# Kernel tuning notes

Hardware: AMD Instinct MI355X
Metric: run time of the kernel (lower is better)

## Reference

```python
import jax, jax.numpy as jnp
import numpy as np

HEADS, DIM_HEAD, LANDMARKS, PINV_ITERS = 8, 64, 256, 6
DIM = 512
KERNEL = 33  # residual depthwise conv kernel size (lucidrains NystromAttention default)
EPS = 1e-5   # torch LayerNorm eps


def setup_inputs() -> dict:
    key = jax.random.key(0)
    ks = jax.random.split(key, 4)
    b, n = 4, 8192  # n divisible by LANDMARKS -> no padding branch
    w = lambda k, shape: jax.random.normal(k, shape, dtype=jnp.float32) * 0.02
    return {
        "x": jax.random.normal(ks[0], (b, n, DIM), dtype=jnp.float32),
        "ln_gamma": jnp.ones((DIM,), jnp.float32),
        "ln_beta": jnp.zeros((DIM,), jnp.float32),
        "w_qkv": w(ks[1], (DIM, 3 * HEADS * DIM_HEAD)),   # to_qkv, no bias
        "w_out": w(ks[2], (HEADS * DIM_HEAD, DIM)),
        "b_out": jnp.zeros((DIM,), jnp.float32),
        "res_kernel": w(ks[3], (HEADS, 1, KERNEL, 1)),    # Conv2d(heads, heads, (33,1), groups=heads)
    }


def _moore_penrose_pinv(a, iters):
    # iterative Moore-Penrose pseudoinverse (lucidrains)
    abs_a = jnp.abs(a)
    col = abs_a.sum(-1).max()  # global max, matching torch.max(col)
    row = abs_a.sum(-2).max()
    z = jnp.swapaxes(a, -1, -2) / (col * row)
    I = jnp.eye(a.shape[-1], dtype=a.dtype)
    for _ in range(iters):
        az = a @ z
        z = 0.25 * z @ (13.0 * I - az @ (15.0 * I - az @ (7.0 * I - az)))
    return z


def reference(x, ln_gamma, ln_beta, w_qkv, w_out, b_out, res_kernel):
    b, n, d = x.shape
    h, dh, m = HEADS, DIM_HEAD, LANDMARKS
    # --- LayerNorm ---
    mu = x.mean(-1, keepdims=True)
    var = ((x - mu) ** 2).mean(-1, keepdims=True)
    xn = (x - mu) * jax.lax.rsqrt(var + EPS) * ln_gamma + ln_beta
    # --- qkv projection ---
    qkv = xn @ w_qkv                                   # (b, n, 3*h*dh)
    q, k, v = jnp.split(qkv, 3, axis=-1)
    to_heads = lambda t: t.reshape(b, n, h, dh).transpose(0, 2, 1, 3)  # (b, h, n, dh)
    q, k, v = to_heads(q), to_heads(k), to_heads(v)
    q = q * (dh ** -0.5)
    # --- landmark pooling (mean over groups of l tokens) ---
    l = n // m
    q_l = q.reshape(b, h, m, l, dh).mean(3)            # (b, h, m, dh)
    k_l = k.reshape(b, h, m, l, dh).mean(3)
    # --- three similarity matrices + softmaxes ---
    attn1 = jax.nn.softmax(jnp.einsum('bhnd,bhmd->bhnm', q, k_l), axis=-1)    # (b,h,n,m)
    attn2 = jax.nn.softmax(jnp.einsum('bhid,bhjd->bhij', q_l, k_l), axis=-1)  # (b,h,m,m)
    attn3 = jax.nn.softmax(jnp.einsum('bhmd,bhnd->bhmn', q_l, k), axis=-1)    # (b,h,m,n)
    out = (attn1 @ _moore_penrose_pinv(attn2, PINV_ITERS)) @ (attn3 @ v)      # (b,h,n,dh)
    # --- depthwise residual conv over sequence dim (groups = heads) ---
    res = jax.lax.conv_general_dilated(
        v, res_kernel, window_strides=(1, 1),
        padding=((KERNEL // 2, KERNEL // 2), (0, 0)),
        dimension_numbers=('NCHW', 'OIHW', 'NCHW'),
        feature_group_count=h)
    out = out + res
    # --- merge heads, output projection, outer residual ---
    out = out.transpose(0, 2, 1, 3).reshape(b, n, h * dh)
    att = out @ w_out + b_out
    return x + att
```

## Files before the change

kernel.cpp:

```cpp
#include <hip/hip_runtime.h>
#include <math.h>

#define NB 4
#define NSEQ 8192
#define DMODEL 512
#define NHEADS 8
#define DHEAD 64
#define NLM 256
#define LTOK 32
#define NBH 32
#define KCONV 33
#define CH3 8

typedef unsigned short bf16_t;
typedef __attribute__((ext_vector_type(8))) short bf16x8;
typedef __attribute__((ext_vector_type(4))) float f32x4;

__device__ __forceinline__ float bf2f(bf16_t u) {
  return __uint_as_float(((unsigned)u) << 16);
}
__device__ __forceinline__ bf16_t f2bf(float f) {
  unsigned u = __float_as_uint(f);
  return (bf16_t)((u + 0x7fffu + ((u >> 16) & 1u)) >> 16);
}
__device__ __forceinline__ void bfpair(unsigned u, float& lo, float& hi) {
  lo = __uint_as_float(u << 16);
  hi = __uint_as_float(u & 0xffff0000u);
}

__global__ __launch_bounds__(256) void ln_kernel(const float* __restrict__ x,
    const float* __restrict__ gamma, const float* __restrict__ beta,
    bf16_t* __restrict__ xn) {
  int row = blockIdx.x * 4 + (threadIdx.x >> 6);
  int lane = threadIdx.x & 63;
  const float4* xr = reinterpret_cast<const float4*>(x + (size_t)row * DMODEL);
  float4 a0 = xr[lane];
  float4 a1 = xr[lane + 64];
  float s  = a0.x + a0.y + a0.z + a0.w + a1.x + a1.y + a1.z + a1.w;
  float s2 = a0.x*a0.x + a0.y*a0.y + a0.z*a0.z + a0.w*a0.w
           + a1.x*a1.x + a1.y*a1.y + a1.z*a1.z + a1.w*a1.w;
  #pragma unroll
  for (int off = 32; off; off >>= 1) {
// ... 215 lines not shown
}

__global__ void colrow_kernel(const float* __restrict__ a2, unsigned int* __restrict__ scal) {
  int bh = blockIdx.x & 31, mode = blockIdx.x >> 5;
  int t = threadIdx.x;
  const float* Ab = a2 + (size_t)bh * NLM * NLM;
  float sum = 0.f;
  if (mode == 0) { for (int j = 0; j < NLM; ++j) sum += fabsf(Ab[(size_t)t * NLM + j]); }
  else           { for (int i2 = 0; i2 < NLM; ++i2) sum += fabsf(Ab[(size_t)i2 * NLM + t]); }
  __shared__ float red[256];
  red[t] = sum; __syncthreads();
  for (int off = 128; off; off >>= 1) { if (t < off) red[t] = fmaxf(red[t], red[t + off]); __syncthreads(); }
  if (t == 0) atomicMax(&scal[mode], __float_as_uint(red[0]));
}

__global__ void zinit_kernel(const float* __restrict__ a2, const unsigned int* __restrict__ scal,
                             bf16_t* __restrict__ zb, bf16_t* __restrict__ a2b) {
  int idx = blockIdx.x * 256 + threadIdx.x;
  float inv = 1.0f / (__uint_as_float(scal[0]) * __uint_as_float(scal[1]));
  int j = idx & 255, i = (idx >> 8) & 255, bh = idx >> 16;
  zb[idx] = f2bf(a2[((size_t)bh * NLM + j) * NLM + i] * inv);
  a2b[idx] = f2bf(a2[idx]);
}

__global__ __launch_bounds__(256) void matmul256_b2b(bf16_t* __restrict__ C,
    const bf16_t* __restrict__ A, const bf16_t* __restrict__ Bm, float s, float alpha) {
  __shared__ __align__(16) bf16_t Ah[64][72];
  __shared__ __align__(16) bf16_t Bh[64][72];
  int bh = blockIdx.y;
  const bf16_t* Ab = A + (size_t)bh * NLM * NLM;
  const bf16_t* Bb = Bm + (size_t)bh * NLM * NLM;
  bf16_t* Cb = C + (size_t)bh * NLM * NLM;
  int rowB = (blockIdx.x >> 2) * 64, colB = (blockIdx.x & 3) * 64;
  int tid = threadIdx.x, w = tid >> 6, lane = tid & 63, tx = lane & 15, g = lane >> 4;
  int jj = tid >> 2, part = tid & 3;
  f32x4 acc[4] = {};
  for (int k0 = 0; k0 < NLM; k0 += 64) {
    {
      const uint4* ar = reinterpret_cast<const uint4*>(
          Ab + (size_t)(rowB + jj) * NLM + k0 + part * 16);
      *reinterpret_cast<uint4*>(&Ah[jj][part * 16]) = ar[0];
      *reinterpret_cast<uint4*>(&Ah[jj][part * 16 + 8]) = ar[1];
      const uint4* br = reinterpret_cast<const uint4*>(
          Bb + (size_t)(k0 + jj) * NLM + colB + part * 16);
      uint4 b0 = br[0], b1 = br[1];
      int d0 = part * 16;
      Bh[d0+ 0][jj] = (bf16_t)(b0.x & 0xffffu); Bh[d0+ 1][jj] = (bf16_t)(b0.x >> 16);
      Bh[d0+ 2][jj] = (bf16_t)(b0.y & 0xffffu); Bh[d0+ 3][jj] = (bf16_t)(b0.y >> 16);
      Bh[d0+ 4][jj] = (bf16_t)(b0.z & 0xffffu); Bh[d0+ 5][jj] = (bf16_t)(b0.z >> 16);
      Bh[d0+ 6][jj] = (bf16_t)(b0.w & 0xffffu); Bh[d0+ 7][jj] = (bf16_t)(b0.w >> 16);
      Bh[d0+ 8][jj] = (bf16_t)(b1.x & 0xffffu); Bh[d0+ 9][jj] = (bf16_t)(b1.x >> 16);
      Bh[d0+10][jj] = (bf16_t)(b1.y & 0xffffu); Bh[d0+11][jj] = (bf16_t)(b1.y >> 16);
      Bh[d0+12][jj] = (bf16_t)(b1.z & 0xffffu); Bh[d0+13][jj] = (bf16_t)(b1.z >> 16);
      Bh[d0+14][jj] = (bf16_t)(b1.w & 0xffffu); Bh[d0+15][jj] = (bf16_t)(b1.w >> 16);
    }
    __syncthreads();
    #pragma unroll
    for (int ks = 0; ks < 2; ++ks) {
      bf16x8 ah = *reinterpret_cast<const bf16x8*>(&Ah[w * 16 + tx][g * 8 + 32 * ks]);
      #pragma unroll
      for (int tn = 0; tn < 4; ++tn) {
        bf16x8 bhf = *reinterpret_cast<const bf16x8*>(&Bh[tn * 16 + tx][g * 8 + 32 * ks]);
        acc[tn] = __builtin_amdgcn_mfma_f32_16x16x32_bf16(ah, bhf, acc[tn], 0, 0, 0);
      }
    }
    __syncthreads();
  }
  #pragma unroll
  for (int tn = 0; tn < 4; ++tn) {
    int c = colB + tn * 16 + tx;
    #pragma unroll
    for (int r = 0; r < 4; ++r) {
      int rr = rowB + w * 16 + g * 4 + r;
      float aij = (s != 0.0f) ? bf2f(Ab[(size_t)rr * NLM + c]) : 0.0f;
      Cb[(size_t)rr * NLM + c] = f2bf(alpha * (s * aij - acc[tn][r]));
    }
  }
}

__global__ __launch_bounds__(256) void matmul256_b2f(float* __restrict__ C,
    const bf16_t* __restrict__ A, const bf16_t* __restrict__ Bm, float s, float alpha) {
  __shared__ __align__(16) bf16_t Ah[64][72];
  __shared__ __align__(16) bf16_t Bh[64][72];
  int bh = blockIdx.y;
  const bf16_t* Ab = A + (size_t)bh * NLM * NLM;
  const bf16_t* Bb = Bm + (size_t)bh * NLM * NLM;
  float* Cb = C + (size_t)bh * NLM * NLM;
  int rowB = (blockIdx.x >> 2) * 64, colB = (blockIdx.x & 3) * 64;
  int tid = threadIdx.x, w = tid >> 6, lane = tid & 63, tx = lane & 15, g = lane >> 4;
  int jj = tid >> 2, part = tid & 3;
  f32x4 acc[4] = {};
  for (int k0 = 0; k0 < NLM; k0 += 64) {
    {
      const uint4* ar = reinterpret_cast<const uint4*>(
          Ab + (size_t)(rowB + jj) * NLM + k0 + part * 16);
      *reinterpret_cast<uint4*>(&Ah[jj][part * 16]) = ar[0];
      *reinterpret_cast<uint4*>(&Ah[jj][part * 16 + 8]) = ar[1];
      const uint4* br = reinterpret_cast<const uint4*>(
          Bb + (size_t)(k0 + jj) * NLM + colB + part * 16);
      uint4 b0 = br[0], b1 = br[1];
      int d0 = part * 16;
      Bh[d0+ 0][jj] = (bf16_t)(b0.x & 0xffffu); Bh[d0+ 1][jj] = (bf16_t)(b0.x >> 16);
      Bh[d0+ 2][jj] = (bf16_t)(b0.y & 0xffffu); Bh[d0+ 3][jj] = (bf16_t)(b0.y >> 16);
      Bh[d0+ 4][jj] = (bf16_t)(b0.z & 0xffffu); Bh[d0+ 5][jj] = (bf16_t)(b0.z >> 16);
      Bh[d0+ 6][jj] = (bf16_t)(b0.w & 0xffffu); Bh[d0+ 7][jj] = (bf16_t)(b0.w >> 16);
      Bh[d0+ 8][jj] = (bf16_t)(b1.x & 0xffffu); Bh[d0+ 9][jj] = (bf16_t)(b1.x >> 16);
      Bh[d0+10][jj] = (bf16_t)(b1.y & 0xffffu); Bh[d0+11][jj] = (bf16_t)(b1.y >> 16);
      Bh[d0+12][jj] = (bf16_t)(b1.z & 0xffffu); Bh[d0+13][jj] = (bf16_t)(b1.z >> 16);
      Bh[d0+14][jj] = (bf16_t)(b1.w & 0xffffu); Bh[d0+15][jj] = (bf16_t)(b1.w >> 16);
    }
    __syncthreads();
    #pragma unroll
    for (int ks = 0; ks < 2; ++ks) {
      bf16x8 ah = *reinterpret_cast<const bf16x8*>(&Ah[w * 16 + tx][g * 8 + 32 * ks]);
      #pragma unroll
      for (int tn = 0; tn < 4; ++tn) {
        bf16x8 bhf = *reinterpret_cast<const bf16x8*>(&Bh[tn * 16 + tx][g * 8 + 32 * ks]);
        acc[tn] = __builtin_amdgcn_mfma_f32_16x16x32_bf16(ah, bhf, acc[tn], 0, 0, 0);
      }
    }
    __syncthreads();
  }
  #pragma unroll
  for (int tn = 0; tn < 4; ++tn) {
    int c = colB + tn * 16 + tx;
    #pragma unroll
    for (int r = 0; r < 4; ++r) {
      int rr = rowB + w * 16 + g * 4 + r;
      float aij = (s != 0.0f) ? bf2f(Ab[(size_t)rr * NLM + c]) : 0.0f;
      Cb[(size_t)rr * NLM + c] = alpha * (s * aij - acc[tn][r]);
    }
  }
}

__global__ __launch_bounds__(256) void matmul256_mfma(float* __restrict__ C,
    const float* __restrict__ A, const float* __restrict__ Bm, float s, float alpha) {
  __shared__ __align__(16) bf16_t Ah[64][72];
  __shared__ __align__(16) bf16_t Al[64][72];
  __shared__ __align__(16) bf16_t Bh[64][72];
  __shared__ __align__(16) bf16_t Bl[64][72];
  int bh = blockIdx.y;
  const float* Ab = A + (size_t)bh * NLM * NLM;
  const float* Bb = Bm + (size_t)bh * NLM * NLM;
  float* Cb = C + (size_t)bh * NLM * NLM;
  int rowB = (blockIdx.x >> 2) * 64, colB = (blockIdx.x & 3) * 64;
  int tid = threadIdx.x, w = tid >> 6, lane = tid & 63, tx = lane & 15, g = lane >> 4;
  f32x4 acc[4] = {};
  for (int k0 = 0; k0 < NLM; k0 += 64) {
    {
      int jj = tid >> 2, part = tid & 3;
      const float* ar = Ab + (size_t)(rowB + jj) * NLM + k0 + part * 16;
      #pragma unroll
      for (int e = 0; e < 16; ++e) {
        float xv = ar[e];
        unsigned u = __float_as_uint(xv);
        Ah[jj][part * 16 + e] = (bf16_t)(u >> 16);
        Al[jj][part * 16 + e] = f2bf(xv - __uint_as_float(u & 0xffff0000u));
      }
      const float* br = Bb + (size_t)(k0 + jj) * NLM + colB + part * 16;
      #pragma unroll
      for (int e = 0; e < 16; ++e) {
        float xv = br[e];
        unsigned u = __float_as_uint(xv);
        Bh[part * 16 + e][jj] = (bf16_t)(u >> 16);
        Bl[part * 16 + e][jj] = f2bf(xv - __uint_as_float(u & 0xffff0000u));
      }
    }
    __syncthreads();
    #pragma unroll
    for (int ks = 0; ks < 2; ++ks) {
      bf16x8 ah = *reinterpret_cast<const bf16x8*>(&Ah[w * 16 + tx][g * 8 + 32 * ks]);
      bf16x8 al = *reinterpret_cast<const bf16x8*>(&Al[w * 16 + tx][g * 8 + 32 * ks]);
      #pragma unroll
      for (int tn = 0; tn < 4; ++tn) {
        bf16x8 bhf = *reinterpret_cast<const bf16x8*>(&Bh[tn * 16 + tx][g * 8 + 32 * ks]);
        bf16x8 blf = *reinterpret_cast<const bf16x8*>(&Bl[tn * 16 + tx][g * 8 + 32 * ks]);
        acc[tn] = __builtin_amdgcn_mfma_f32_16x16x32_bf16(ah, bhf, acc[tn], 0, 0, 0);
        acc[tn] = __builtin_amdgcn_mfma_f32_16x16x32_bf16(ah, blf, acc[tn], 0, 0, 0);
        acc[tn] = __builtin_amdgcn_mfma_f32_16x16x32_bf16(al, bhf, acc[tn], 0, 0, 0);
      }
    }
    __syncthreads();
  }
  #pragma unroll
  for (int tn = 0; tn < 4; ++tn) {
    int c = colB + tn * 16 + tx;
    #pragma unroll
    for (int r = 0; r < 4; ++r) {
      int rr = rowB + w * 16 + g * 4 + r;
      float aij = (s != 0.0f) ? Ab[(size_t)rr * NLM + c] : 0.0f;
      Cb[(size_t)rr * NLM + c] = alpha * (s * aij - acc[tn][r]);
    }
  }
}

__global__ __launch_bounds__(256) void attn3v_mfma(const bf16_t* __restrict__ qlb,
    const bf16_t* __restrict__ k, const bf16_t* __restrict__ vT,
    float* __restrict__ Wpart, float* __restrict__ mlpart) {
  __shared__ __align__(16) bf16_t Qs[64][72];
  __shared__ __align__(16) bf16_t Ks[64][72];
  __shared__ __align__(16) bf16_t Vt[64][72];
  __shared__ __align__(16) bf16_t Ps[64][72];
  int chunk = blockIdx.x, lmt = blockIdx.y, bh = blockIdx.z;
  int tid = threadIdx.x;
  int w = tid >> 6, lane = tid & 63;
  int tx = lane & 15, g = lane >> 4;
  int lm0 = lmt * 64;
  int jj = tid >> 2, part = tid & 3;
  {
    const uint4* qr = reinterpret_cast<const uint4*>(
        qlb + ((size_t)bh * NLM + lm0 + jj) * DHEAD + part * 16);
    *reinterpret_cast<uint4*>(&Qs[jj][part * 16]) = qr[0];
    *reinterpret_cast<uint4*>(&Qs[jj][part * 16 + 8]) = qr[1];
  }
  f32x4 oacc[4] = {};
  float lreg[4] = {0.f, 0.f, 0.f, 0.f};
  const bf16_t* kb = k + (size_t)bh * NSEQ * DHEAD;
  const bf16_t* vtb = vT + (size_t)bh * DHEAD * NSEQ + (size_t)jj * NSEQ;
  __syncthreads();
  for (int it = 0; it < NSEQ / (CH3 * 64); ++it) {
    int n0 = chunk * (NSEQ / CH3) + it * 64;
    {
      const uint4* kr = reinterpret_cast<const uint4*>(kb + (size_t)(n0 + jj) * DHEAD + part * 16);
      *reinterpret_cast<uint4*>(&Ks[jj][part * 16]) = kr[0];
      *reinterpret_cast<uint4*>(&Ks[jj][part * 16 + 8]) = kr[1];
      const uint4* vr = reinterpret_cast<const uint4*>(vtb + n0 + part * 16);
      *reinterpret_cast<uint4*>(&Vt[jj][part * 16]) = vr[0];
      *reinterpret_cast<uint4*>(&Vt[jj][part * 16 + 8]) = vr[1];
    }
    __syncthreads();
    f32x4 sacc[4] = {};
    bf16x8 aq0 = *reinterpret_cast<const bf16x8*>(&Qs[w * 16 + tx][g * 8]);
    bf16x8 aq1 = *reinterpret_cast<const bf16x8*>(&Qs[w * 16 + tx][g * 8 + 32]);
    #pragma unroll
    for (int tn = 0; tn < 4; ++tn) {
      bf16x8 bk0 = *reinterpret_cast<const bf16x8*>(&Ks[tn * 16 + tx][g * 8]);
      bf16x8 bk1 = *reinterpret_cast<const bf16x8*>(&Ks[tn * 16 + tx][g * 8 + 32]);
      sacc[tn] = __builtin_amdgcn_mfma_f32_16x16x32_bf16(aq0, bk0, sacc[tn], 0, 0, 0);
      sacc[tn] = __builtin_amdgcn_mfma_f32_16x16x32_bf16(aq1, bk1, sacc[tn], 0, 0, 0);
    }
    #pragma unroll
    for (int r = 0; r < 4; ++r) {
      float p0 = __expf(sacc[0][r]);
      float p1 = __expf(sacc[1][r]);
      float p2 = __expf(sacc[2][r]);
      float p3 = __expf(sacc[3][r]);
      float ts = p0 + p1 + p2 + p3;
      #pragma unroll
      for (int off = 1; off < 16; off <<= 1) ts += __shfl_xor(ts, off);
      lreg[r] += ts;
      int prow = w * 16 + g * 4 + r;
      Ps[prow][tx]      = f2bf(p0);
      Ps[prow][tx + 16] = f2bf(p1);
      Ps[prow][tx + 32] = f2bf(p2);
      Ps[prow][tx + 48] = f2bf(p3);
    }
    __syncthreads();
    bf16x8 ap0 = *reinterpret_cast<const bf16x8*>(&Ps[w * 16 + tx][g * 8]);
    bf16x8 ap1 = *reinterpret_cast<const bf16x8*>(&Ps[w * 16 + tx][g * 8 + 32]);
    #pragma unroll
    for (int td = 0; td < 4; ++td) {
      bf16x8 bv0 = *reinterpret_cast<const bf16x8*>(&Vt[td * 16 + tx][g * 8]);
      bf16x8 bv1 = *reinterpret_cast<const bf16x8*>(&Vt[td * 16 + tx][g * 8 + 32]);
      oacc[td] = __builtin_amdgcn_mfma_f32_16x16x32_bf16(ap0, bv0, oacc[td], 0, 0, 0);
      oacc[td] = __builtin_amdgcn_mfma_f32_16x16x32_bf16(ap1, bv1, oacc[td], 0, 0, 0);
    }
    __syncthreads();
  }
  #pragma unroll
  for (int r = 0; r < 4; ++r) {
    size_t ob = ((size_t)(chunk * NBH + bh) * NLM + lm0 + w * 16 + g * 4 + r);
    #pragma unroll
    for (int td = 0; td < 4; ++td)
      Wpart[ob * DHEAD + tx + 16 * td] = oacc[td][r];
    if (tx == 0) { mlpart[ob * 2] = 0.f; mlpart[ob * 2 + 1] = lreg[r]; }
  }
}

// ... 4 lines not shown
  int s0 = idx >> 6;
  const int CHS = NBH * NLM;
  float M = -1e30f;
  #pragma unroll
  for (int c = 0; c < CH3; ++c) M = fmaxf(M, mlpart[((size_t)c * CHS + s0) * 2]);
  float L = 0.f, wv = 0.f;
  #pragma unroll
  for (int c = 0; c < CH3; ++c) {
    float e = __expf(mlpart[((size_t)c * CHS + s0) * 2] - M);
    L += mlpart[((size_t)c * CHS + s0) * 2 + 1] * e;
    wv += Wpart[((size_t)c * CHS + s0) * DHEAD + d] * e;
  }
  Wm[idx] = wv / L;
}

__global__ void zw_kernel(const float* __restrict__ z, const float* __restrict__ W,
                          bf16_t* __restrict__ Ub) {
  int idx = blockIdx.x * 256 + threadIdx.x;
  int d = idx & 63, i = (idx >> 6) & 255, bh = idx >> 14;
  const float* zr = z + ((size_t)bh * NLM + i) * NLM;
  const float* Wb = W + (size_t)bh * NLM * DHEAD + d;
  float acc = 0.f;
  for (int j = 0; j < NLM; ++j) acc += zr[j] * Wb[(size_t)j * DHEAD];
  Ub[idx] = f2bf(acc);
}

__global__ __launch_bounds__(256) void attn1_mfma(const bf16_t* __restrict__ q,
    const bf16_t* __restrict__ klb, const bf16_t* __restrict__ Ut,
    bf16_t* __restrict__ outp) {
  __shared__ __align__(16) bf16_t Qs[64][72];
  __shared__ __align__(16) bf16_t Ks[64][72];
  __shared__ __align__(16) bf16_t Vt[64][72];
  __shared__ __align__(16) bf16_t Ps[64][72];
  int nt = blockIdx.x, bh = blockIdx.y;
  int tid = threadIdx.x;
  int w = tid >> 6, lane = tid & 63;
  int tx = lane & 15, g = lane >> 4;
  int n0 = nt * 64;
  int b = bh >> 3, h = bh & 7;
  int jj = tid >> 2, part = tid & 3;
  {
    const uint4* qr = reinterpret_cast<const uint4*>(
        q + ((size_t)bh * NSEQ + n0 + jj) * DHEAD + part * 16);
    *reinterpret_cast<uint4*>(&Qs[jj][part * 16]) = qr[0];
    *reinterpret_cast<uint4*>(&Qs[jj][part * 16 + 8]) = qr[1];
  }
  f32x4 oacc[4] = {};
  float lreg[4] = {0.f, 0.f, 0.f, 0.f};
  const bf16_t* utb = Ut + (size_t)bh * DHEAD * NLM + (size_t)jj * NLM;
  __syncthreads();
  for (int it = 0; it < 4; ++it) {
    int lm0 = it * 64;
    {
      const uint4* kr = reinterpret_cast<const uint4*>(
          klb + ((size_t)bh * NLM + lm0 + jj) * DHEAD + part * 16);
      *reinterpret_cast<uint4*>(&Ks[jj][part * 16]) = kr[0];
      *reinterpret_cast<uint4*>(&Ks[jj][part * 16 + 8]) = kr[1];
      const uint4* ur = reinterpret_cast<const uint4*>(utb + lm0 + part * 16);
      *reinterpret_cast<uint4*>(&Vt[jj][part * 16]) = ur[0];
      *reinterpret_cast<uint4*>(&Vt[jj][part * 16 + 8]) = ur[1];
    }
    __syncthreads();
    f32x4 sacc[4] = {};
    bf16x8 aq0 = *reinterpret_cast<const bf16x8*>(&Qs[w * 16 + tx][g * 8]);
    bf16x8 aq1 = *reinterpret_cast<const bf16x8*>(&Qs[w * 16 + tx][g * 8 + 32]);
    #pragma unroll
    for (int tn = 0; tn < 4; ++tn) {
      bf16x8 bk0 = *reinterpret_cast<const bf16x8*>(&Ks[tn * 16 + tx][g * 8]);
      bf16x8 bk1 = *reinterpret_cast<const bf16x8*>(&Ks[tn * 16 + tx][g * 8 + 32]);
      sacc[tn] = __builtin_amdgcn_mfma_f32_16x16x32_bf16(aq0, bk0, sacc[tn], 0, 0, 0);
      sacc[tn] = __builtin_amdgcn_mfma_f32_16x16x32_bf16(aq1, bk1, sacc[tn], 0, 0, 0);
    }
    #pragma unroll
    for (int r = 0; r < 4; ++r) {
      float p0 = __expf(sacc[0][r]);
      float p1 = __expf(sacc[1][r]);
      float p2 = __expf(sacc[2][r]);
      float p3 = __expf(sacc[3][r]);
      float ts = p0 + p1 + p2 + p3;
      #pragma unroll
      for (int off = 1; off < 16; off <<= 1) ts += __shfl_xor(ts, off);
      lreg[r] += ts;
      int prow = w * 16 + g * 4 + r;
      Ps[prow][tx]      = f2bf(p0);
      Ps[prow][tx + 16] = f2bf(p1);
      Ps[prow][tx + 32] = f2bf(p2);
      Ps[prow][tx + 48] = f2bf(p3);
    }
    __syncthreads();
    bf16x8 ap0 = *reinterpret_cast<const bf16x8*>(&Ps[w * 16 + tx][g * 8]);
    bf16x8 ap1 = *reinterpret_cast<const bf16x8*>(&Ps[w * 16 + tx][g * 8 + 32]);
    #pragma unroll
    for (int td = 0; td < 4; ++td) {
      bf16x8 bv0 = *reinterpret_cast<const bf16x8*>(&Vt[td * 16 + tx][g * 8]);
      bf16x8 bv1 = *reinterpret_cast<const bf16x8*>(&Vt[td * 16 + tx][g * 8 + 32]);
      oacc[td] = __builtin_amdgcn_mfma_f32_16x16x32_bf16(ap0, bv0, oacc[td], 0, 0, 0);
      oacc[td] = __builtin_amdgcn_mfma_f32_16x16x32_bf16(ap1, bv1, oacc[td], 0, 0, 0);
    }
    __syncthreads();
  }
  #pragma unroll
  for (int r = 0; r < 4; ++r) {
    float inv = 1.0f / lreg[r];
    int n = n0 + w * 16 + g * 4 + r;
    #pragma unroll
    for (int td = 0; td < 4; ++td)
      outp[((size_t)(b * NSEQ + n)) * DMODEL + h * DHEAD + tx + 16 * td] =
          f2bf(oacc[td][r] * inv);
  }
}
// ... 34 lines not shown
  const float* x     = (const float*)d_in[0];
  const float* gamma = (const float*)d_in[1];
  const float* beta  = (const float*)d_in[2];
  const float* wqkv  = (const float*)d_in[3];
  const float* wout  = (const float*)d_in[4];
  const float* bout  = (const float*)d_in[5];
  const float* rk    = (const float*)d_in[6];
  float* y = (float*)d_out;

  char* wsb = (char*)d_ws;
  bf16_t* xn = (bf16_t*)(wsb);
  bf16_t* q  = (bf16_t*)(wsb + 33554432ull);
  bf16_t* k  = (bf16_t*)(wsb + 67108864ull);
  bf16_t* v  = (bf16_t*)(wsb + 100663296ull);
  float* a2f = (float*)(wsb + 134217728ull);
  float* z5  = (float*)(wsb + 142606336ull);
  bf16_t* a2b = (bf16_t*)(wsb + 150994944ull);
  bf16_t* zb  = (bf16_t*)(wsb + 155189248ull);
  bf16_t* azb = (bf16_t*)(wsb + 159383552ull);
  bf16_t* t1b = (bf16_t*)(wsb + 163577856ull);
  bf16_t* t2b = (bf16_t*)(wsb + 167772160ull);
  float* azf = (float*)(wsb + 150994944ull);
  float* t2f = (float*)(wsb + 159383552ull);
  float* t1f = (float*)(wsb + 167772160ull);
  float* zf  = (float*)(wsb + 150994944ull);
  float* ql  = (float*)(wsb + 176160768ull);
  float* kl  = (float*)(wsb + 178257920ull);
  float* Wm  = (float*)(wsb + 180355072ull);
  bf16_t* Ub = (bf16_t*)(wsb + 182452224ull);
  unsigned int* scal = (unsigned int*)(wsb + 184549376ull);
  bf16_t* wqkvT = (bf16_t*)(wsb + 182452224ull);
  bf16_t* woutT = (bf16_t*)(wsb + 184549440ull);
  bf16_t* qlb = (bf16_t*)(wsb + 185073728ull);
  bf16_t* klb = (bf16_t*)(wsb + 186122304ull);
  bf16_t* Ut  = (bf16_t*)(wsb + 187170880ull);

  bf16_t* vT = xn;
  float* Wpart  = a2f;
  float* mlpart = t1f;
  bf16_t* out_pre = (bf16_t*)(wsb + 134217728ull);

  castT_kernel<<<3072, 256, 0, stream>>>(wqkv, wqkvT, 1536, 1);
  castT_kernel<<<1024, 256, 0, stream>>>(wout, woutT, 512, 0);
  ln_kernel<<<8192, 256, 0, stream>>>(x, gamma, beta, xn);
  gemm_qkv_mfma<<<dim3(256, 12), 256, 0, stream>>>(xn, wqkvT, q, k, v);
  transpose64_kernel<<<dim3(128, 32), 256, 0, stream>>>(v, vT, NSEQ);
  pool_kernel<<<4096, 256, 0, stream>>>(q, k, ql, kl, qlb, klb);
  attn2_kernel<<<dim3(256, 32), 256, 0, stream>>>(ql, kl, a2f);
  zero2_kernel<<<1, 64, 0, stream>>>(scal);
  colrow_kernel<<<64, 256, 0, stream>>>(a2f, scal);
  zinit_kernel<<<8192, 256, 0, stream>>>(a2f, scal, zb, a2b);

  bf16_t *pzb = zb, *pt2b = t2b;
  for (int it = 0; it < 4; ++it) {
    matmul256_b2b<<<dim3(16, 32), 256, 0, stream>>>(azb, a2b, pzb, 0.f, -1.f);
    matmul256_b2b<<<dim3(16, 32), 256, 0, stream>>>(pt2b, azb, azb, 7.f, 1.f);
    matmul256_b2b<<<dim3(16, 32), 256, 0, stream>>>(t1b, azb, pt2b, 15.f, 1.f);
    matmul256_b2b<<<dim3(16, 32), 256, 0, stream>>>(pt2b, pzb, t1b, 13.f, 0.25f);
    bf16_t* tmp = pzb; pzb = pt2b; pt2b = tmp;
  }
  matmul256_b2b<<<dim3(16, 32), 256, 0, stream>>>(azb, a2b, pzb, 0.f, -1.f);
  matmul256_b2b<<<dim3(16, 32), 256, 0, stream>>>(pt2b, azb, azb, 7.f, 1.f);
  matmul256_b2b<<<dim3(16, 32), 256, 0, stream>>>(t1b, azb, pt2b, 15.f, 1.f);
  matmul256_b2f<<<dim3(16, 32), 256, 0, stream>>>(z5, pzb, t1b, 13.f, 0.25f);
  matmul256_mfma<<<dim3(16, 32), 256, 0, stream>>>(azf, a2f, z5, 0.f, -1.f);
  matmul256_mfma<<<dim3(16, 32), 256, 0, stream>>>(t2f, azf, azf, 7.f, 1.f);
  matmul256_mfma<<<dim3(16, 32), 256, 0, stream>>>(t1f, azf, t2f, 15.f, 1.f);
  matmul256_mfma<<<dim3(16, 32), 256, 0, stream>>>(zf, z5, t1f, 13.f, 0.25f);

  attn3v_mfma<<<dim3(CH3, 4, 32), 256, 0, stream>>>(qlb, k, vT, Wpart, mlpart);
  attn3v_combine<<<2048, 256, 0, stream>>>(Wpart, mlpart, Wm);
  zw_kernel<<<2048, 256, 0, stream>>>(zf, Wm, Ub);
  transpose64_kernel<<<dim3(4, 32), 256, 0, stream>>>(Ub, Ut, NLM);
  attn1_mfma<<<dim3(128, 32), 256, 0, stream>>>(q, klb, Ut, out_pre);
  conv_kernel<<<8192, 256, 0, stream>>>(v, rk, out_pre);
  gemm_out_mfma<<<dim3(256, 4), 256, 0, stream>>>(out_pre, woutT, bout, x, y);
}
```

Before: 707.4 us.

## Reformulate pinv iteration on symmetric Y=A·Aᵀ products and drop LDS staging

Rewrites the Newton–Schulz pseudoinverse so it iterates on products of a2 with its own transpose (Y and M matrices) instead of az/z. This lets matmuls read both operands row-major directly from global memory, with no transposed LDS staging, and pairs two independent GEMMs per launch through grid z. The final z is recovered as aᵀ·M·W through two small kernels that fold in the scale factor. The attn3v and attn1 kernels also drop their LDS staging of Q, K and V tiles and load MFMA fragments straight from global memory. The risks are more uncoalesced global traffic and different numerical behaviour in bf16.

```diff
diff --git a/kernel.cpp b/kernel.cpp
--- a/kernel.cpp
+++ b/kernel.cpp
@@ -26,6 +26,17 @@
 __device__ __forceinline__ void bfpair(unsigned u, float& lo, float& hi) {
   lo = __uint_as_float(u << 16);
   hi = __uint_as_float(u & 0xffff0000u);
+}
+__device__ __forceinline__ void split8(const float* p, bf16x8& hi, bf16x8& lo) {
+  float4 f0 = *reinterpret_cast<const float4*>(p);
+  float4 f1 = *reinterpret_cast<const float4*>(p + 4);
+  float f[8] = {f0.x, f0.y, f0.z, f0.w, f1.x, f1.y, f1.z, f1.w};
+  #pragma unroll
+  for (int i = 0; i < 8; ++i) {
+    unsigned u = __float_as_uint(f[i]);
+    hi[i] = (short)(u >> 16);
+    lo[i] = (short)f2bf(f[i] - __uint_as_float(u & 0xffff0000u));
+  }
 }
 
 __global__ __launch_bounds__(256) void ln_kernel(const float* __restrict__ x,
@@ -271,112 +282,77 @@
   if (t == 0) atomicMax(&scal[mode], __float_as_uint(red[0]));
 }
 
-__global__ void zinit_kernel(const float* __restrict__ a2, const unsigned int* __restrict__ scal,
-                             bf16_t* __restrict__ zb, bf16_t* __restrict__ a2b) {
+__global__ void a2cast_kernel(const float* __restrict__ a2, bf16_t* __restrict__ a2b) {
   int idx = blockIdx.x * 256 + threadIdx.x;
-  float inv = 1.0f / (__uint_as_float(scal[0]) * __uint_as_float(scal[1]));
-  int j = idx & 255, i = (idx >> 8) & 255, bh = idx >> 16;
-  zb[idx] = f2bf(a2[((size_t)bh * NLM + j) * NLM + i] * inv);
   a2b[idx] = f2bf(a2[idx]);
 }
 
-__global__ __launch_bounds__(256) void matmul256_b2b(bf16_t* __restrict__ C,
-    const bf16_t* __restrict__ A, const bf16_t* __restrict__ Bm, float s, float alpha) {
-  __shared__ __align__(16) bf16_t Ah[64][72];
-  __shared__ __align__(16) bf16_t Bh[64][72];
+__global__ __launch_bounds__(256) void mmsym_bb(
+    bf16_t* __restrict__ C0, const bf16_t* __restrict__ A0,
+    bf16_t* __restrict__ C1, const bf16_t* __restrict__ A1,
+    const bf16_t* __restrict__ B,
+    const bf16_t* __restrict__ Yel, const bf16_t* __restrict__ Y2el,
+    const unsigned int* __restrict__ scal, int mode) {
   int bh = blockIdx.y;
-  const bf16_t* Ab = A + (size_t)bh * NLM * NLM;
-  const bf16_t* Bb = Bm + (size_t)bh * NLM * NLM;
-  bf16_t* Cb = C + (size_t)bh * NLM * NLM;
+  size_t base = (size_t)bh * NLM * NLM;
+  const bf16_t* A = (blockIdx.z == 0) ? A0 : A1;
+  bf16_t* C = (blockIdx.z == 0) ? C0 : C1;
   int rowB = (blockIdx.x >> 2) * 64, colB = (blockIdx.x & 3) * 64;
   int tid = threadIdx.x, w = tid >> 6, lane = tid & 63, tx = lane & 15, g = lane >> 4;
-  int jj = tid >> 2, part = tid & 3;
+  const bf16_t* arow = A + base + (size_t)(rowB + w * 16 + tx) * NLM + g * 8;
+  const bf16_t* brow = B + base + (size_t)(colB + tx) * NLM + g * 8;
   f32x4 acc[4] = {};
-  for (int k0 = 0; k0 < NLM; k0 += 64) {
-    {
-      const uint4* ar = reinterpret_cast<const uint4*>(
-          Ab + (size_t)(rowB + jj) * NLM + k0 + part * 16);
-      *reinterpret_cast<uint4*>(&Ah[jj][part * 16]) = ar[0];
-      *reinterpret_cast<uint4*>(&Ah[jj][part * 16 + 8]) = ar[1];
-      const uint4* br = reinterpret_cast<const uint4*>(
-          Bb + (size_t)(k0 + jj) * NLM + colB + part * 16);
-      uint4 b0 = br[0], b1 = br[1];
-      int d0 = part * 16;
-      Bh[d0+ 0][jj] = (bf16_t)(b0.x & 0xffffu); Bh[d0+ 1][jj] = (bf16_t)(b0.x >> 16);
-      Bh[d0+ 2][jj] = (bf16_t)(b0.y & 0xffffu); Bh[d0+ 3][jj] = (bf16_t)(b0.y >> 16);
-      Bh[d0+ 4][jj] = (bf16_t)(b0.z & 0xffffu); Bh[d0+ 5][jj] = (bf16_t)(b0.z >> 16);
-      Bh[d0+ 6][jj] = (bf16_t)(b0.w & 0xffffu); Bh[d0+ 7][jj] = (bf16_t)(b0.w >> 16);
-      Bh[d0+ 8][jj] = (bf16_t)(b1.x & 0xffffu); Bh[d0+ 9][jj] = (bf16_t)(b1.x >> 16);
-      Bh[d0+10][jj] = (bf16_t)(b1.y & 0xffffu); Bh[d0+11][jj] = (bf16_t)(b1.y >> 16);
-      Bh[d0+12][jj] = (bf16_t)(b1.z & 0xffffu); Bh[d0+13][jj] = (bf16_t)(b1.z >> 16);
-      Bh[d0+14][jj] = (bf16_t)(b1.w & 0xffffu); Bh[d0+15][jj] = (bf16_t)(b1.w >> 16);
-    }
-    __syncthreads();
-    #pragma unroll
-    for (int ks = 0; ks < 2; ++ks) {
-      bf16x8 ah = *reinterpret_cast<const bf16x8*>(&Ah[w * 16 + tx][g * 8 + 32 * ks]);
-      #pragma unroll
-      for (int tn = 0; tn < 4; ++tn) {
-        bf16x8 bhf = *reinterpret_cast<const bf16x8*>(&Bh[tn * 16 + tx][g * 8 + 32 * ks]);
-        acc[tn] = __builtin_amdgcn_mfma_f32_16x16x32_bf16(ah, bhf, acc[tn], 0, 0, 0);
-      }
-    }
-    __syncthreads();
-  }
+  #pragma unroll
+  for (int ks = 0; ks < 8; ++ks) {
+    bf16x8 af = *reinterpret_cast<const bf16x8*>(arow + ks * 32);
+    #pragma unroll
+    for (int tn = 0; tn < 4; ++tn) {
+      bf16x8 bfv = *reinterpret_cast<const bf16x8*>(brow + (size_t)(tn * 16) * NLM + ks * 32);
+      acc[tn] = __builtin_amdgcn_mfma_f32_16x16x32_bf16(af, bfv, acc[tn], 0, 0, 0);
+    }
+  }
+  float mult = 1.0f;
+  if (scal) mult = 1.0f / (__uint_as_float(scal[0]) * __uint_as_float(scal[1]));
   #pragma unroll
   for (int tn = 0; tn < 4; ++tn) {
     int c = colB + tn * 16 + tx;
     #pragma unroll
     for (int r = 0; r < 4; ++r) {
       int rr = rowB + w * 16 + g * 4 + r;
-      float aij = (s != 0.0f) ? bf2f(Ab[(size_t)rr * NLM + c]) : 0.0f;
-      Cb[(size_t)rr * NLM + c] = f2bf(alpha * (s * aij - acc[tn][r]));
-    }
-  }
-}
-
-__global__ __launch_bounds__(256) void matmul256_b2f(float* __restrict__ C,
-    const bf16_t* __restrict__ A, const bf16_t* __restrict__ Bm, float s, float alpha) {
-  __shared__ __align__(16) bf16_t Ah[64][72];
-  __shared__ __align__(16) bf16_t Bh[64][72];
+      float v = acc[tn][r];
+      if (mode == 1) {
+        float yv = bf2f(Yel[base + (size_t)rr * NLM + c]);
+        float y2v = bf2f(Y2el[base + (size_t)rr * NLM + c]);
+        v = 0.25f * (((rr == c) ? 13.f : 0.f) - 15.f * yv + 7.f * y2v - v);
+      } else {
+        v *= mult;
+      }
+      C[base + (size_t)rr * NLM + c] = f2bf(v);
+    }
+  }
+}
+
+__global__ __launch_bounds__(256) void mmsym_bf(
+    float* __restrict__ C0, const bf16_t* __restrict__ A0,
+    float* __restrict__ C1, const bf16_t* __restrict__ A1,
+    const bf16_t* __restrict__ B) {
   int bh = blockIdx.y;
-  const bf16_t* Ab = A + (size_t)bh * NLM * NLM;
-  const bf16_t* Bb = Bm + (size_t)bh * NLM * NLM;
-  float* Cb = C + (size_t)bh * NLM * NLM;
+  size_t base = (size_t)bh * NLM * NLM;
+  const bf16_t* A = (blockIdx.z == 0) ? A0 : A1;
+  float* C = (blockIdx.z == 0) ? C0 : C1;
   int rowB = (blockIdx.x >> 2) * 64, colB = (blockIdx.x & 3) * 64;
   int tid = threadIdx.x, w = tid >> 6, lane = tid & 63, tx = lane & 15, g = lane >> 4;
-  int jj = tid >> 2, part = tid & 3;
+  const bf16_t* arow = A + base + (size_t)(rowB + w * 16 + tx) * NLM + g * 8;
+  const bf16_t* brow = B + base + (size_t)(colB + tx) * NLM + g * 8;
   f32x4 acc[4] = {};
-  for (int k0 = 0; k0 < NLM; k0 += 64) {
-    {
-      const uint4* ar = reinterpret_cast<const uint4*>(
-          Ab + (size_t)(rowB + jj) * NLM + k0 + part * 16);
-      *reinterpret_cast<uint4*>(&Ah[jj][part * 16]) = ar[0];
-      *reinterpret_cast<uint4*>(&Ah[jj][part * 16 + 8]) = ar[1];
-      const uint4* br = reinterpret_cast<const uint4*>(
-          Bb + (size_t)(k0 + jj) * NLM + colB + part * 16);
-      uint4 b0 = br[0], b1 = br[1];
-      int d0 = part * 16;
-      Bh[d0+ 0][jj] = (bf16_t)(b0.x & 0xffffu); Bh[d0+ 1][jj] = (bf16_t)(b0.x >> 16);
-      Bh[d0+ 2][jj] = (bf16_t)(b0.y & 0xffffu); Bh[d0+ 3][jj] = (bf16_t)(b0.y >> 16);
-      Bh[d0+ 4][jj] = (bf16_t)(b0.z & 0xffffu); Bh[d0+ 5][jj] = (bf16_t)(b0.z >> 16);
-      Bh[d0+ 6][jj] = (bf16_t)(b0.w & 0xffffu); Bh[d0+ 7][jj] = (bf16_t)(b0.w >> 16);
-      Bh[d0+ 8][jj] = (bf16_t)(b1.x & 0xffffu); Bh[d0+ 9][jj] = (bf16_t)(b1.x >> 16);
-      Bh[d0+10][jj] = (bf16_t)(b1.y & 0xffffu); Bh[d0+11][jj] = (bf16_t)(b1.y >> 16);
-      Bh[d0+12][jj] = (bf16_t)(b1.z & 0xffffu); Bh[d0+13][jj] = (bf16_t)(b1.z >> 16);
-      Bh[d0+14][jj] = (bf16_t)(b1.w & 0xffffu); Bh[d0+15][jj] = (bf16_t)(b1.w >> 16);
-    }
-    __syncthreads();
-    #pragma unroll
-    for (int ks = 0; ks < 2; ++ks) {
-      bf16x8 ah = *reinterpret_cast<const bf16x8*>(&Ah[w * 16 + tx][g * 8 + 32 * ks]);
-      #pragma unroll
-      for (int tn = 0; tn < 4; ++tn) {
-        bf16x8 bhf = *reinterpret_cast<const bf16x8*>(&Bh[tn * 16 + tx][g * 8 + 32 * ks]);
-        acc[tn] = __builtin_amdgcn_mfma_f32_16x16x32_bf16(ah, bhf, acc[tn], 0, 0, 0);
-      }
-    }
-    __syncthreads();
+  #pragma unroll
+  for (int ks = 0; ks < 8; ++ks) {
+    bf16x8 af = *reinterpret_cast<const bf16x8*>(arow + ks * 32);
+    #pragma unroll
+    for (int tn = 0; tn < 4; ++tn) {
+      bf16x8 bfv = *reinterpret_cast<const bf16x8*>(brow + (size_t)(tn * 16) * NLM + ks * 32);
+      acc[tn] = __builtin_amdgcn_mfma_f32_16x16x32_bf16(af, bfv, acc[tn], 0, 0, 0);
+    }
   }
   #pragma unroll
   for (int tn = 0; tn < 4; ++tn) {
@@ -384,60 +360,33 @@
     #pragma unroll
     for (int r = 0; r < 4; ++r) {
       int rr = rowB + w * 16 + g * 4 + r;
-      float aij = (s != 0.0f) ? bf2f(Ab[(size_t)rr * NLM + c]) : 0.0f;
-      Cb[(size_t)rr * NLM + c] = alpha * (s * aij - acc[tn][r]);
-    }
-  }
-}
-
-__global__ __launch_bounds__(256) void matmul256_mfma(float* __restrict__ C,
-    const float* __restrict__ A, const float* __restrict__ Bm, float s, float alpha) {
-  __shared__ __align__(16) bf16_t Ah[64][72];
-  __shared__ __align__(16) bf16_t Al[64][72];
-  __shared__ __align__(16) bf16_t Bh[64][72];
-  __shared__ __align__(16) bf16_t Bl[64][72];
+      C[base + (size_t)rr * NLM + c] = acc[tn][r];
+    }
+  }
+}
+
+__global__ __launch_bounds__(256) void mmsym_ff(
+    float* __restrict__ C, const float* __restrict__ A, const float* __restrict__ B,
+    const float* __restrict__ Yel, const float* __restrict__ Y2el, int mode) {
   int bh = blockIdx.y;
-  const float* Ab = A + (size_t)bh * NLM * NLM;
-  const float* Bb = Bm + (size_t)bh * NLM * NLM;
-  float* Cb = C + (size_t)bh * NLM * NLM;
+  size_t base = (size_t)bh * NLM * NLM;
   int rowB = (blockIdx.x >> 2) * 64, colB = (blockIdx.x & 3) * 64;
   int tid = threadIdx.x, w = tid >> 6, lane = tid & 63, tx = lane & 15, g = lane >> 4;
+  const float* arow = A + base + (size_t)(rowB + w * 16 + tx) * NLM + g * 8;
+  const float* brow = B + base + (size_t)(colB + tx) * NLM + g * 8;
   f32x4 acc[4] = {};
-  for (int k0 = 0; k0 < NLM; k0 += 64) {
-    {
-      int jj = tid >> 2, part = tid & 3;
-      const float* ar = Ab + (size_t)(rowB + jj) * NLM + k0 + part * 16;
-      #pragma unroll
-      for (int e = 0; e < 16; ++e) {
-        float xv = ar[e];
-        unsigned u = __float_as_uint(xv);
-        Ah[jj][part * 16 + e] = (bf16_t)(u >> 16);
-        Al[jj][part * 16 + e] = f2bf(xv - __uint_as_float(u & 0xffff0000u));
-      }
-      const float* br = Bb + (size_t)(k0 + jj) * NLM + colB + part * 16;
-      #pragma unroll
-      for (int e = 0; e < 16; ++e) {
-        float xv = br[e];
-        unsigned u = __float_as_uint(xv);
-        Bh[part * 16 + e][jj] = (bf16_t)(u >> 16);
-        Bl[part * 16 + e][jj] = f2bf(xv - __uint_as_float(u & 0xffff0000u));
-      }
-    }
-    __syncthreads();
-    #pragma unroll
-    for (int ks = 0; ks < 2; ++ks) {
-      bf16x8 ah = *reinterpret_cast<const bf16x8*>(&Ah[w * 16 + tx][g * 8 + 32 * ks]);
-      bf16x8 al = *reinterpret_cast<const bf16x8*>(&Al[w * 16 + tx][g * 8 + 32 * ks]);
-      #pragma unroll
-      for (int tn = 0; tn < 4; ++tn) {
-        bf16x8 bhf = *reinterpret_cast<const bf16x8*>(&Bh[tn * 16 + tx][g * 8 + 32 * ks]);
-        bf16x8 blf = *reinterpret_cast<const bf16x8*>(&Bl[tn * 16 + tx][g * 8 + 32 * ks]);
-        acc[tn] = __builtin_amdgcn_mfma_f32_16x16x32_bf16(ah, bhf, acc[tn], 0, 0, 0);
-        acc[tn] = __builtin_amdgcn_mfma_f32_16x16x32_bf16(ah, blf, acc[tn], 0, 0, 0);
-        acc[tn] = __builtin_amdgcn_mfma_f32_16x16x32_bf16(al, bhf, acc[tn], 0, 0, 0);
-      }
-    }
-    __syncthreads();
+  #pragma unroll
+  for (int ks = 0; ks < 8; ++ks) {
+    bf16x8 ah, al;
+    split8(arow + ks * 32, ah, al);
+    #pragma unroll
+    for (int tn = 0; tn < 4; ++tn) {
+      bf16x8 bh_, bl_;
+      split8(brow + (size_t)(tn * 16) * NLM + ks * 32, bh_, bl_);
+      acc[tn] = __builtin_amdgcn_mfma_f32_16x16x32_bf16(ah, bh_, acc[tn], 0, 0, 0);
+      acc[tn] = __builtin_amdgcn_mfma_f32_16x16x32_bf16(ah, bl_, acc[tn], 0, 0, 0);
+      acc[tn] = __builtin_amdgcn_mfma_f32_16x16x32_bf16(al, bh_, acc[tn], 0, 0, 0);
+    }
   }
   #pragma unroll
   for (int tn = 0; tn < 4; ++tn) {
@@ -445,8 +394,13 @@
     #pragma unroll
     for (int r = 0; r < 4; ++r) {
       int rr = rowB + w * 16 + g * 4 + r;
-      float aij = (s != 0.0f) ? Ab[(size_t)rr * NLM + c] : 0.0f;
-      Cb[(size_t)rr * NLM + c] = alpha * (s * aij - acc[tn][r]);
+      float v = acc[tn][r];
+      if (mode == 1) {
+        float yv = Yel[base + (size_t)rr * NLM + c];
+        float y2v = Y2el[base + (size_t)rr * NLM + c];
+        v = 0.25f * (((rr == c) ? 13.f : 0.f) - 15.f * yv + 7.f * y2v - v);
+      }
+      C[base + (size_t)rr * NLM + c] = v;
     }
   }
 }
@@ -454,45 +408,25 @@
 __global__ __launch_bounds__(256) void attn3v_mfma(const bf16_t* __restrict__ qlb,
     const bf16_t* __restrict__ k, const bf16_t* __restrict__ vT,
     float* __restrict__ Wpart, float* __restrict__ mlpart) {
-  __shared__ __align__(16) bf16_t Qs[64][72];
-  __shared__ __align__(16) bf16_t Ks[64][72];
-  __shared__ __align__(16) bf16_t Vt[64][72];
   __shared__ __align__(16) bf16_t Ps[64][72];
   int chunk = blockIdx.x, lmt = blockIdx.y, bh = blockIdx.z;
-  int tid = threadIdx.x;
-  int w = tid >> 6, lane = tid & 63;
-  int tx = lane & 15, g = lane >> 4;
+  int tid = threadIdx.x, w = tid >> 6, lane = tid & 63, tx = lane & 15, g = lane >> 4;
   int lm0 = lmt * 64;
-  int jj = tid >> 2, part = tid & 3;
-  {
-    const uint4* qr = reinterpret_cast<const uint4*>(
-        qlb + ((size_t)bh * NLM + lm0 + jj) * DHEAD + part * 16);
-    *reinterpret_cast<uint4*>(&Qs[jj][part * 16]) = qr[0];
-    *reinterpret_cast<uint4*>(&Qs[jj][part * 16 + 8]) = qr[1];
-  }
+  const bf16_t* qrow = qlb + ((size_t)bh * NLM + lm0 + w * 16 + tx) * DHEAD + g * 8;
+  bf16x8 aq0 = *reinterpret_cast<const bf16x8*>(qrow);
+  bf16x8 aq1 = *reinterpret_cast<const bf16x8*>(qrow + 32);
+  const bf16_t* kb = k + (size_t)bh * NSEQ * DHEAD;
+  const bf16_t* vtb = vT + (size_t)bh * DHEAD * NSEQ;
   f32x4 oacc[4] = {};
   float lreg[4] = {0.f, 0.f, 0.f, 0.f};
-  const bf16_t* kb = k + (size_t)bh * NSEQ * DHEAD;
-  const bf16_t* vtb = vT + (size_t)bh * DHEAD * NSEQ + (size_t)jj * NSEQ;
-  __syncthreads();
   for (int it = 0; it < NSEQ / (CH3 * 64); ++it) {
     int n0 = chunk * (NSEQ / CH3) + it * 64;
-    {
-      const uint4* kr = reinterpret_cast<const uint4*>(kb + (size_t)(n0 + jj) * DHEAD + part * 16);
-      *reinterpret_cast<uint4*>(&Ks[jj][part * 16]) = kr[0];
-      *reinterpret_cast<uint4*>(&Ks[jj][part * 16 + 8]) = kr[1];
-      const uint4* vr = reinterpret_cast<const uint4*>(vtb + n0 + part * 16);
-      *reinterpret_cast<uint4*>(&Vt[jj][part * 16]) = vr[0];
-      *reinterpret_cast<uint4*>(&Vt[jj][part * 16 + 8]) = vr[1];
-    }
-    __syncthreads();
     f32x4 sacc[4] = {};
-    bf16x8 aq0 = *reinterpret_cast<const bf16x8*>(&Qs[w * 16 + tx][g * 8]);
-    bf16x8 aq1 = *reinterpret_cast<const bf16x8*>(&Qs[w * 16 + tx][g * 8 + 32]);
     #pragma unroll
     for (int tn = 0; tn < 4; ++tn) {
-      bf16x8 bk0 = *reinterpret_cast<const bf16x8*>(&Ks[tn * 16 + tx][g * 8]);
-      bf16x8 bk1 = *reinterpret_cast<const bf16x8*>(&Ks[tn * 16 + tx][g * 8 + 32]);
+      const bf16_t* krow = kb + (size_t)(n0 + tn * 16 + tx) * DHEAD + g * 8;
+      bf16x8 bk0 = *reinterpret_cast<const bf16x8*>(krow);
+      bf16x8 bk1 = *reinterpret_cast<const bf16x8*>(krow + 32);
       sacc[tn] = __builtin_amdgcn_mfma_f32_16x16x32_bf16(aq0, bk0, sacc[tn], 0, 0, 0);
       sacc[tn] = __builtin_amdgcn_mfma_f32_16x16x32_bf16(aq1, bk1, sacc[tn], 0, 0, 0);
     }
@@ -517,8 +451,9 @@
     bf16x8 ap1 = *reinterpret_cast<const bf16x8*>(&Ps[w * 16 + tx][g * 8 + 32]);
     #pragma unroll
     for (int td = 0; td < 4; ++td) {
-      bf16x8 bv0 = *reinterpret_cast<const bf16x8*>(&Vt[td * 16 + tx][g * 8]);
-      bf16x8 bv1 = *reinterpret_cast<const bf16x8*>(&Vt[td * 16 + tx][g * 8 + 32]);
+      const bf16_t* vrow = vtb + (size_t)(td * 16 + tx) * NSEQ + n0 + g * 8;
+      bf16x8 bv0 = *reinterpret_cast<const bf16x8*>(vrow);
+      bf16x8 bv1 = *reinterpret_cast<const bf16x8*>(vrow + 32);
       oacc[td] = __builtin_amdgcn_mfma_f32_16x16x32_bf16(ap0, bv0, oacc[td], 0, 0, 0);
       oacc[td] = __builtin_amdgcn_mfma_f32_16x16x32_bf16(ap1, bv1, oacc[td], 0, 0, 0);
     }
@@ -553,60 +488,52 @@
   Wm[idx] = wv / L;
 }
 
-__global__ void zw_kernel(const float* __restrict__ z, const float* __restrict__ W,
-                          bf16_t* __restrict__ Ub) {
+__global__ void rk_kernel(const float* __restrict__ M6, const float* __restrict__ Wm,
+                          float* __restrict__ R) {
   int idx = blockIdx.x * 256 + threadIdx.x;
   int d = idx & 63, i = (idx >> 6) & 255, bh = idx >> 14;
-  const float* zr = z + ((size_t)bh * NLM + i) * NLM;
-  const float* Wb = W + (size_t)bh * NLM * DHEAD + d;
+  const float* mr = M6 + (size_t)bh * NLM * NLM + (size_t)i * NLM;
+  const float* wb = Wm + (size_t)bh * NLM * DHEAD + d;
   float acc = 0.f;
-  for (int j = 0; j < NLM; ++j) acc += zr[j] * Wb[(size_t)j * DHEAD];
-  Ub[idx] = f2bf(acc);
+  for (int j = 0; j < NLM; ++j) acc += mr[j] * wb[(size_t)j * DHEAD];
+  R[idx] = acc;
+}
+
+__global__ void uk_kernel(const float* __restrict__ a2f, const float* __restrict__ R,
+                          const unsigned int* __restrict__ scal, bf16_t* __restrict__ Ub) {
+  int idx = blockIdx.x * 256 + threadIdx.x;
+  int d = idx & 63, i = (idx >> 6) & 255, bh = idx >> 14;
+  float inv = 1.0f / (__uint_as_float(scal[0]) * __uint_as_float(scal[1]));
+  const float* ac = a2f + (size_t)bh * NLM * NLM + i;
+  const float* rb = R + (size_t)bh * NLM * DHEAD + d;
+  float acc = 0.f;
+  for (int j = 0; j < NLM; ++j) acc += ac[(size_t)j * NLM] * rb[(size_t)j * DHEAD];
+  Ub[idx] = f2bf(acc * inv);
 }
 
 __global__ __launch_bounds__(256) void attn1_mfma(const bf16_t* __restrict__ q,
     const bf16_t* __restrict__ klb, const bf16_t* __restrict__ Ut,
     bf16_t* __restrict__ outp) {
-  __shared__ __align__(16) bf16_t Qs[64][72];
-  __shared__ __align__(16) bf16_t Ks[64][72];
-  __shared__ __align__(16) bf16_t Vt[64][72];
   __shared__ __align__(16) bf16_t Ps[64][72];
   int nt = blockIdx.x, bh = blockIdx.y;
-  int tid = threadIdx.x;
-  int w = tid >> 6, lane = tid & 63;
-  int tx = lane & 15, g = lane >> 4;
+  int tid = threadIdx.x, w = tid >> 6, lane = tid & 63, tx = lane & 15, g = lane >> 4;
   int n0 = nt * 64;
   int b = bh >> 3, h = bh & 7;
-  int jj = tid >> 2, part = tid & 3;
-  {
-    const uint4* qr = reinterpret_cast<const uint4*>(
-        q + ((size_t)bh * NSEQ + n0 + jj) * DHEAD + part * 16);
-    *reinterpret_cast<uint4*>(&Qs[jj][part * 16]) = qr[0];
-    *reinterpret_cast<uint4*>(&Qs[jj][part * 16 + 8]) = qr[1];
-  }
+  const bf16_t* qrow = q + ((size_t)bh * NSEQ + n0 + w * 16 + tx) * DHEAD + g * 8;
+  bf16x8 aq0 = *reinterpret_cast<const bf16x8*>(qrow);
+  bf16x8 aq1 = *reinterpret_cast<const bf16x8*>(qrow + 32);
+  const bf16_t* klbb = klb + (size_t)bh * NLM * DHEAD;
+  const bf16_t* utb = Ut + (size_t)bh * DHEAD * NLM;
   f32x4 oacc[4] = {};
   float lreg[4] = {0.f, 0.f, 0.f, 0.f};
-  const bf16_t* utb = Ut + (size_t)bh * DHEAD * NLM + (size_t)jj * NLM;
-  __syncthreads();
   for (int it = 0; it < 4; ++it) {
     int lm0 = it * 64;
-    {
-      const uint4* kr = reinterpret_cast<const uint4*>(
-          klb + ((size_t)bh * NLM + lm0 + jj) * DHEAD + part * 16);
-      *reinterpret_cast<uint4*>(&Ks[jj][part * 16]) = kr[0];
-      *reinterpret_cast<uint4*>(&Ks[jj][part * 16 + 8]) = kr[1];
-      const uint4* ur = reinterpret_cast<const uint4*>(utb + lm0 + part * 16);
-      *reinterpret_cast<uint4*>(&Vt[jj][part * 16]) = ur[0];
-      *reinterpret_cast<uint4*>(&Vt[jj][part * 16 + 8]) = ur[1];
-    }
-    __syncthreads();
     f32x4 sacc[4] = {};
-    bf16x8 aq0 = *reinterpret_cast<const bf16x8*>(&Qs[w * 16 + tx][g * 8]);
-    bf16x8 aq1 = *reinterpret_cast<const bf16x8*>(&Qs[w * 16 + tx][g * 8 + 32]);
     #pragma unroll
     for (int tn = 0; tn < 4; ++tn) {
-      bf16x8 bk0 = *reinterpret_cast<const bf16x8*>(&Ks[tn * 16 + tx][g * 8]);
-      bf16x8 bk1 = *reinterpret_cast<const bf16x8*>(&Ks[tn * 16 + tx][g * 8 + 32]);
+      const bf16_t* krow = klbb + (size_t)(lm0 + tn * 16 + tx) * DHEAD + g * 8;
+      bf16x8 bk0 = *reinterpret_cast<const bf16x8*>(krow);
+      bf16x8 bk1 = *reinterpret_cast<const bf16x8*>(krow + 32);
       sacc[tn] = __builtin_amdgcn_mfma_f32_16x16x32_bf16(aq0, bk0, sacc[tn], 0, 0, 0);
       sacc[tn] = __builtin_amdgcn_mfma_f32_16x16x32_bf16(aq1, bk1, sacc[tn], 0, 0, 0);
     }
@@ -631,8 +558,9 @@
     bf16x8 ap1 = *reinterpret_cast<const bf16x8*>(&Ps[w * 16 + tx][g * 8 + 32]);
     #pragma unroll
     for (int td = 0; td < 4; ++td) {
-      bf16x8 bv0 = *reinterpret_cast<const bf16x8*>(&Vt[td * 16 + tx][g * 8]);
-      bf16x8 bv1 = *reinterpret_cast<const bf16x8*>(&Vt[td * 16 + tx][g * 8 + 32]);
+      const bf16_t* urow = utb + (size_t)(td * 16 + tx) * NLM + lm0 + g * 8;
+      bf16x8 bv0 = *reinterpret_cast<const bf16x8*>(urow);
+      bf16x8 bv1 = *reinterpret_cast<const bf16x8*>(urow + 32);
       oacc[td] = __builtin_amdgcn_mfma_f32_16x16x32_bf16(ap0, bv0, oacc[td], 0, 0, 0);
       oacc[td] = __builtin_amdgcn_mfma_f32_16x16x32_bf16(ap1, bv1, oacc[td], 0, 0, 0);
     }
@@ -697,16 +625,21 @@
   bf16_t* k  = (bf16_t*)(wsb + 67108864ull);
   bf16_t* v  = (bf16_t*)(wsb + 100663296ull);
   float* a2f = (float*)(wsb + 134217728ull);
-  float* z5  = (float*)(wsb + 142606336ull);
-  bf16_t* a2b = (bf16_t*)(wsb + 150994944ull);
-  bf16_t* zb  = (bf16_t*)(wsb + 155189248ull);
-  bf16_t* azb = (bf16_t*)(wsb + 159383552ull);
-  bf16_t* t1b = (bf16_t*)(wsb + 163577856ull);
-  bf16_t* t2b = (bf16_t*)(wsb + 167772160ull);
-  float* azf = (float*)(wsb + 150994944ull);
-  float* t2f = (float*)(wsb + 159383552ull);
-  float* t1f = (float*)(wsb + 167772160ull);
-  float* zf  = (float*)(wsb + 150994944ull);
+  bf16_t* YA  = (bf16_t*)(wsb + 142606336ull);
+  bf16_t* MA  = (bf16_t*)(wsb + 146800640ull);
+  bf16_t* YB  = (bf16_t*)(wsb + 150994944ull);
+  bf16_t* MB  = (bf16_t*)(wsb + 155189248ull);
+  bf16_t* Y2b = (bf16_t*)(wsb + 159383552ull);
+  bf16_t* pb  = (bf16_t*)(wsb + 163577856ull);
+  bf16_t* a2b = (bf16_t*)(wsb + 167772160ull);
+  float* M5f = (float*)(wsb + 167772160ull);
+  float* Y5f = (float*)(wsb + 150994944ull);
+  float* Y2f = (float*)(wsb + 142606336ull);
+  float* pf  = (float*)(wsb + 159383552ull);
+  float* M6f = (float*)(wsb + 142606336ull);
+  float* Wpart  = (float*)(wsb + 150994944ull);
+  float* mlpart = (float*)(wsb + 167772160ull);
+  float* Rm     = (float*)(wsb + 168820736ull);
   float* ql  = (float*)(wsb + 176160768ull);
   float* kl  = (float*)(wsb + 178257920ull);
   float* Wm  = (float*)(wsb + 180355072ull);
@@ -719,8 +652,6 @@
   bf16_t* Ut  = (bf16_t*)(wsb + 187170880ull);
 
   bf16_t* vT = xn;
-  float* Wpart  = a2f;
-  float* mlpart = t1f;
   bf16_t* out_pre = (bf16_t*)(wsb + 134217728ull);
 
   castT_kernel<<<3072, 256, 0, stream>>>(wqkv, wqkvT, 1536, 1);
@@ -732,28 +663,33 @@
   attn2_kernel<<<dim3(256, 32), 256, 0, stream>>>(ql, kl, a2f);
   zero2_kernel<<<1, 64, 0, stream>>>(scal);
   colrow_kernel<<<64, 256, 0, stream>>>(a2f, scal);
-  zinit_kernel<<<8192, 256, 0, stream>>>(a2f, scal, zb, a2b);
-
-  bf16_t *pzb = zb, *pt2b = t2b;
-  for (int it = 0; it < 4; ++it) {
-    matmul256_b2b<<<dim3(16, 32), 256, 0, stream>>>(azb, a2b, pzb, 0.f, -1.f);
-    matmul256_b2b<<<dim3(16, 32), 256, 0, stream>>>(pt2b, azb, azb, 7.f, 1.f);
-    matmul256_b2b<<<dim3(16, 32), 256, 0, stream>>>(t1b, azb, pt2b, 15.f, 1.f);
-    matmul256_b2b<<<dim3(16, 32), 256, 0, stream>>>(pt2b, pzb, t1b, 13.f, 0.25f);
-    bf16_t* tmp = pzb; pzb = pt2b; pt2b = tmp;
-  }
-  matmul256_b2b<<<dim3(16, 32), 256, 0, stream>>>(azb, a2b, pzb, 0.f, -1.f);
-  matmul256_b2b<<<dim3(16, 32), 256, 0, stream>>>(pt2b, azb, azb, 7.f, 1.f);
-  matmul256_b2b<<<dim3(16, 32), 256, 0, stream>>>(t1b, azb, pt2b, 15.f, 1.f);
-  matmul256_b2f<<<dim3(16, 32), 256, 0, stream>>>(z5, pzb, t1b, 13.f, 0.25f);
-  matmul256_mfma<<<dim3(16, 32), 256, 0, stream>>>(azf, a2f, z5, 0.f, -1.f);
-  matmul256_mfma<<<dim3(16, 32), 256, 0, stream>>>(t2f, azf, azf, 7.f, 1.f);
-  matmul256_mfma<<<dim3(16, 32), 256, 0, stream>>>(t1f, azf, t2f, 15.f, 1.f);
-  matmul256_mfma<<<dim3(16, 32), 256, 0, stream>>>(zf, z5, t1f, 13.f, 0.25f);
+  a2cast_kernel<<<8192, 256, 0, stream>>>(a2f, a2b);
+
+  dim3 g1(16, 32, 1), g2(16, 32, 2);
+  mmsym_bb<<<g1, 256, 0, stream>>>(YA, a2b, nullptr, nullptr, a2b, nullptr, nullptr, scal, 0);
+  mmsym_bb<<<g1, 256, 0, stream>>>(Y2b, YA, nullptr, nullptr, YA, nullptr, nullptr, nullptr, 0);
+  mmsym_bb<<<g1, 256, 0, stream>>>(MB, YA, nullptr, nullptr, Y2b, YA, Y2b, nullptr, 1);
+  mmsym_bb<<<g1, 256, 0, stream>>>(YB, YA, nullptr, nullptr, MB, nullptr, nullptr, nullptr, 0);
+  bf16_t *Yc = YB, *Mc = MB, *Yn = YA, *Mn = MA;
+  for (int it = 1; it <= 3; ++it) {
+    mmsym_bb<<<g1, 256, 0, stream>>>(Y2b, Yc, nullptr, nullptr, Yc, nullptr, nullptr, nullptr, 0);
+    mmsym_bb<<<g1, 256, 0, stream>>>(pb, Yc, nullptr, nullptr, Y2b, Yc, Y2b, nullptr, 1);
+    mmsym_bb<<<g2, 256, 0, stream>>>(Mn, Mc, Yn, Yc, pb, nullptr, nullptr, nullptr, 0);
+    bf16_t* t;
+    t = Yc; Yc = Yn; Yn = t;
+    t = Mc; Mc = Mn; Mn = t;
+  }
+  mmsym_bb<<<g1, 256, 0, stream>>>(Y2b, Yc, nullptr, nullptr, Yc, nullptr, nullptr, nullptr, 0);
+  mmsym_bb<<<g1, 256, 0, stream>>>(pb, Yc, nullptr, nullptr, Y2b, Yc, Y2b, nullptr, 1);
+  mmsym_bf<<<g2, 256, 0, stream>>>(M5f, Mc, Y5f, Yc, pb);
+  mmsym_ff<<<g1, 256, 0, stream>>>(Y2f, Y5f, Y5f, nullptr, nullptr, 0);
+  mmsym_ff<<<g1, 256, 0, stream>>>(pf, Y5f, Y2f, Y5f, Y2f, 1);
+  mmsym_ff<<<g1, 256, 0, stream>>>(M6f, M5f, pf, nullptr, nullptr, 0);
 
   attn3v_mfma<<<dim3(CH3, 4, 32), 256, 0, stream>>>(qlb, k, vT, Wpart, mlpart);
   attn3v_combine<<<2048, 256, 0, stream>>>(Wpart, mlpart, Wm);
-  zw_kernel<<<2048, 256, 0, stream>>>(zf, Wm, Ub);
+  rk_kernel<<<2048, 256, 0, stream>>>(M6f, Wm, Rm);
+  uk_kernel<<<2048, 256, 0, stream>>>(a2f, Rm, scal, Ub);
   transpose64_kernel<<<dim3(4, 32), 256, 0, stream>>>(Ub, Ut, NLM);
   attn1_mfma<<<dim3(128, 32), 256, 0, stream>>>(q, klb, Ut, out_pre);
   conv_kernel<<<8192, 256, 0, stream>>>(v, rk, out_pre);
```

Result: slower. 944.6 us (+33.5%).
